# Optimization experiments

Hardware: AMD Instinct MI355X
Metric: run time of the kernel (lower is better)

Reference implementation:

```python
import jax, jax.numpy as jnp
import numpy as np

N = 100000        # nodes
E = 3200000       # edges per support (avg degree 32)
D_IN, D_OUT = 256, 128
ATT_H = 32
ALPHA, BETA = 0.5, 0.5  # FLAGS.alpha / FLAGS.beta


def setup_inputs() -> dict:
    key = jax.random.key(0)
    ks = jax.random.split(key, 10)
    x = jax.random.normal(ks[0], (N, D_IN), dtype=jnp.float32)
    glorot = lambda k, shp: jax.random.uniform(k, shp, jnp.float32,
                                               -np.sqrt(6.0 / sum(shp)), np.sqrt(6.0 / sum(shp)))
    Wa = glorot(ks[1], (D_IN, D_OUT))
    Wb = glorot(ks[2], (D_IN, D_OUT))
    Wc = glorot(ks[3], (D_IN, D_OUT))
    attn_w1 = glorot(ks[4], (D_OUT, ATT_H))
    attn_b1 = jnp.zeros((ATT_H,), jnp.float32)
    attn_w2 = glorot(ks[5], (ATT_H, 1))
    rows = jax.random.randint(ks[6], (7, E), 0, N, dtype=jnp.int32)
    cols = jax.random.randint(ks[7], (7, E), 0, N, dtype=jnp.int32)
    # normalized-adjacency-like positive values, scaled ~1/degree
    vals = jax.random.uniform(ks[8], (7, E), jnp.float32) * (1.0 / 32.0)
    return {"x": x, "Wa": Wa, "Wb": Wb, "Wc": Wc,
            "attn_w1": attn_w1, "attn_b1": attn_b1, "attn_w2": attn_w2,
            "rows": rows, "cols": cols, "vals": vals}


def reference(x, Wa, Wb, Wc, attn_w1, attn_b1, attn_w2, rows, cols, vals):
    n = x.shape[0]

    def spmm(i, X):
        # support[i] @ X via COO gather-scale-scatter: memory-bound SpMM
        return jax.ops.segment_sum(vals[i][:, None] * X[cols[i]], rows[i], num_segments=n)

    def bilinear_pooling(i, X):
        s = spmm(i, X)
        return 0.5 * (s * s - spmm(i, X * X))

    pre_a = x @ Wa                    # [N, D_OUT]
    pre_b = x @ Wb
    _ = x @ Wc                        # computed in original, never used
    sec_ord = 0.5 * (pre_a * pre_a - pre_a * pre_b)
    pre_al = pre_a + sec_ord

    emb = jnp.stack([pre_a, pre_al], axis=1)          # [N, 2, D_OUT]
    h = jnp.tanh(emb @ attn_w1 + attn_b1)             # [N, 2, 32]
    att = jax.nn.softmax(h @ attn_w2, axis=1)         # [N, 2, 1]
    pre_sup = jnp.sum(att * emb, axis=1)              # [N, D_OUT]

    out_gcn = spmm(0, pre_sup)
    out_bi1 = spmm(5, bilinear_pooling(1, pre_sup) - bilinear_pooling(3, pre_sup))
    out_bi2 = spmm(6, bilinear_pooling(2, pre_sup) - bilinear_pooling(4, pre_sup))
    out_bi = (1.0 - BETA) * out_bi1 + BETA * out_bi2
    output = (1.0 - ALPHA) * out_gcn + ALPHA * out_bi
    return jax.nn.relu(output)
```

## Files before the change

kernel.cpp:

```cpp
#include <hip/hip_runtime.h>

typedef unsigned int uint;
typedef unsigned short ushort;

__device__ __forceinline__ float bfl(uint u){ return __uint_as_float(u << 16); }
__device__ __forceinline__ float bfh(uint u){ return __uint_as_float(u & 0xFFFF0000u); }
__device__ __forceinline__ uint f2bfbits(float f){
    uint b = __float_as_uint(f);
    return (b + 0x7FFFu + ((b >> 16) & 1u)) >> 16;
}
__device__ __forceinline__ uint packbf2(float a, float b){
    return f2bfbits(a) | (f2bfbits(b) << 16);
}
__device__ __forceinline__ int smap(int4 m, int s){
    return (s == 0) ? m.x : (s == 1) ? m.y : (s == 2) ? m.z : m.w;
}
__device__ __forceinline__ int2 ldnt(const int2* p){
    long long v = __builtin_nontemporal_load((const long long*)p);
    int2 r; r.x = (int)(v & 0xFFFFFFFFll); r.y = (int)(v >> 32); return r;
}

#define CH 6144
#define SBSHIFT 7
#define SBROWS 128
#define HISTP 784
#define SBUF_CAP 5120
#define PGRID 2048


#define BM 64
#define BK 32
__global__ __launch_bounds__(256) void gemm_kernel(const float* __restrict__ x,
                                                   const float* __restrict__ Wa,
                                                   const float* __restrict__ Wb,
                                                   float* __restrict__ AB, int N) {
    __shared__ float xsT[BK][BM + 4];
    __shared__ float wsm[BK][256];
    int t = threadIdx.x;
    int rowbase = blockIdx.x * BM;
    int tx = t & 15, ty = t >> 4;
    float acc[4][16];
    #pragma unroll
    for (int i = 0; i < 4; i++)
        #pragma unroll
        for (int j = 0; j < 16; j++) acc[i][j] = 0.f;

    for (int k0 = 0; k0 < 256; k0 += BK) {
        {
            int r = t & 63;
            int koff = (t >> 6) * 8;
            int gr = rowbase + r; if (gr >= N) gr = N - 1;
            const float* src = x + (size_t)gr * 256 + k0 + koff;
            float4 u0 = *(const float4*)(src);
            float4 u1 = *(const float4*)(src + 4);
            xsT[koff + 0][r] = u0.x; xsT[koff + 1][r] = u0.y;
            xsT[koff + 2][r] = u0.z; xsT[koff + 3][r] = u0.w;
            xsT[koff + 4][r] = u1.x; xsT[koff + 5][r] = u1.y;
            xsT[koff + 6][r] = u1.z; xsT[koff + 7][r] = u1.w;
        }
        {
            #pragma unroll
            for (int i = 0; i < 8; i++) {
                int f = t + i * 256;
                int rr = f >> 6, c4 = f & 63;
                const float* src = (c4 < 32) ? &Wa[(size_t)(k0 + rr) * 128 + c4 * 4]
                                             : &Wb[(size_t)(k0 + rr) * 128 + (c4 - 32) * 4];
                *(float4*)&wsm[rr][c4 * 4] = *(const float4*)src;
            }
        }
        __syncthreads();
        #pragma unroll
        for (int kk = 0; kk < BK; ++kk) {
            float4 a = *(const float4*)&xsT[kk][ty * 4];
            float av[4] = {a.x, a.y, a.z, a.w};
            float bv[16];
            #pragma unroll
            for (int q = 0; q < 4; q++)
                *(float4*)&bv[q * 4] = *(const float4*)&wsm[kk][q * 64 + tx * 4];
            #pragma unroll
            for (int i = 0; i < 4; i++)
                #pragma unroll
                for (int j = 0; j < 16; j++)
                    acc[i][j] = fmaf(av[i], bv[j], acc[i][j]);
        }
        __syncthreads();
    }
    #pragma unroll
    for (int i = 0; i < 4; i++) {
        int gr = rowbase + ty * 4 + i;
        if (gr < N) {
            #pragma unroll
            for (int q = 0; q < 4; q++) {
                float4 o = {acc[i][q*4], acc[i][q*4+1], acc[i][q*4+2], acc[i][q*4+3]};
                *(float4*)&AB[(size_t)gr * 256 + q * 64 + tx * 4] = o;
            }
        }
    }
}

__global__ __launch_bounds__(256) void attn_kernel(const float* __restrict__ AB,
        const float* __restrict__ w1, const float* __restrict__ b1,
        const float* __restrict__ w2, uint* __restrict__ Pb, int N) {
    __shared__ float w1s[128 * 32];
    __shared__ float b1s[32], w2s[32];
    __shared__ float aS[4][128], alS[4][128];
    int t = threadIdx.x;
    #pragma unroll
    for (int i = 0; i < 16; i++) w1s[t + i * 256] = w1[t + i * 256];
    if (t < 32) { b1s[t] = b1[t]; w2s[t] = w2[t]; }

    int w = t >> 6, lane = t & 63;
    int node = blockIdx.x * 4 + w;
    bool active = node < N;
    int nclamp = active ? node : (N - 1);
    float2 a = *(const float2*)(AB + (size_t)nclamp * 256 + lane * 2);
    float2 b = *(const float2*)(AB + (size_t)nclamp * 256 + 128 + lane * 2);
    float2 al;
    al.x = a.x + 0.5f * (a.x * a.x - a.x * b.x);
    al.y = a.y + 0.5f * (a.y * a.y - a.y * b.y);
    aS[w][lane * 2] = a.x;   aS[w][lane * 2 + 1] = a.y;
    alS[w][lane * 2] = al.x; alS[w][lane * 2 + 1] = al.y;
    __syncthreads();

    int j = lane & 31;
    const float* src = (lane < 32) ? aS[w] : alS[w];
    float acc = b1s[j];
    #pragma unroll 8
    for (int d = 0; d < 128; ++d) acc = fmaf(src[d], w1s[d * 32 + j], acc);
    float h = tanhf(acc);
    float prod = h * w2s[j];
    #pragma unroll
    for (int off = 1; off < 32; off <<= 1) prod += __shfl_xor(prod, off);
    float eo = __shfl_xor(prod, 32);
    float e0 = (lane < 32) ? prod : eo;
    float e1 = (lane < 32) ? eo : prod;
    float m = fmaxf(e0, e1);
    float p0 = expf(e0 - m), p1 = expf(e1 - m);
    float inv = 1.0f / (p0 + p1);
    float at0 = p0 * inv, at1 = p1 * inv;
    if (active) {
        float px = at0 * a.x + at1 * al.x;
        float py = at0 * a.y + at1 * al.y;
        Pb[(size_t)node * 64 + lane] = packbf2(px, py);
    }
}


__device__ __forceinline__ void block_scan1024(int* a, int t, int* wsum) {
    int lane = t & 63, wid = t >> 6;
    int c0 = a[t * 4], c1 = a[t * 4 + 1], c2 = a[t * 4 + 2], c3 = a[t * 4 + 3];
    int tsum = c0 + c1 + c2 + c3, incl = tsum;
    #pragma unroll
    for (int off = 1; off < 64; off <<= 1) {
        int y = __shfl_up(incl, off);
        if (lane >= off) incl += y;
    }
    if (lane == 63) wsum[wid] = incl;
    __syncthreads();
    int wb = 0;
    #pragma unroll
    for (int w = 0; w < 4; w++) if (w < wid) wb += wsum[w];
    int excl = wb + incl - tsum;
    a[t * 4] = excl; a[t * 4 + 1] = excl + c0;
    a[t * 4 + 2] = excl + c0 + c1; a[t * 4 + 3] = excl + c0 + c1 + c2;
    __syncthreads();
}

__global__ __launch_bounds__(256) void count_chunk(const int* __restrict__ rows, int4 map,
        int* __restrict__ lenTab, int* __restrict__ gtot, int NSB, int nchunks, int E) {
    __shared__ int hist[HISTP];
    int c = blockIdx.x, s = blockIdx.y, t = threadIdx.x;
    size_t sb = (size_t)smap(map, s) * E;
    int e0 = c * CH, e1 = e0 + CH; if (e1 > E) e1 = E;
    for (int i = t; i < HISTP; i += 256) hist[i] = 0;
    __syncthreads();
    for (int e = e0 + t; e < e1; e += 256)
        atomicAdd(&hist[(uint)rows[sb + e] >> SBSHIFT], 1);
    __syncthreads();
    for (int b = t; b < NSB; b += 256) {
        int l = hist[b];
        lenTab[((size_t)s * NSB + b) * nchunks + c] = l;
        if (l) atomicAdd(&gtot[s * NSB + b], l);
    }
}

__global__ __launch_bounds__(256) void bucket_scanex(const int* __restrict__ gtot,
        int* __restrict__ bbase, int NSB) {
    __shared__ int a[1024];
    __shared__ int wsum[4];
    int s = blockIdx.x, t = threadIdx.x;
    #pragma unroll
    for (int k = 0; k < 4; k++) {
        int i = t + k * 256;
        a[i] = (i < NSB) ? gtot[s * NSB + i] : 0;
    }
    __syncthreads();
    block_scan1024(a, t, wsum);
    #pragma unroll
    for (int k = 0; k < 4; k++) {
        int i = t + k * 256;
        if (i <= NSB) bbase[s * (NSB + 1) + i] = a[i];
    }
}

__global__ __launch_bounds__(64) void pos_scan(const int* __restrict__ lenTab,
        const int* __restrict__ bbase, int* __restrict__ segPos, int NSB, int nchunks) {
    int b = blockIdx.x, s = blockIdx.y, lane = threadIdx.x;
    const int* lt = lenTab + ((size_t)s * NSB + b) * nchunks;
    int* sp = segPos + ((size_t)s * NSB + b) * nchunks;
    int run = bbase[s * (NSB + 1) + b];
    for (int c0 = 0; c0 < nchunks; c0 += 64) {
        int c = c0 + lane;
        int v = (c < nchunks) ? lt[c] : 0;
        int incl = v;
        #pragma unroll
        for (int off = 1; off < 64; off <<= 1) {
            int y = __shfl_up(incl, off);
            if (lane >= off) incl += y;
        }
        if (c < nchunks) sp[c] = run + incl - v;
        run += __shfl(incl, 63);
    }
}

__global__ __launch_bounds__(256) void place_chunk(const int* __restrict__ rows,
        const int* __restrict__ cols, const float* __restrict__ vals, int4 map,
        const int* __restrict__ segPos, int2* __restrict__ stage2,
        int NSB, int nchunks, int E) {
    __shared__ int2 sbuf[CH];
    __shared__ ushort bmap[CH];
    __shared__ int cur[1024];
    __shared__ int off[1024];
    __shared__ int spos[HISTP];
    __shared__ int wsum[4];
    int c = blockIdx.x, s = blockIdx.y, t = threadIdx.x;
    size_t sb = (size_t)smap(map, s) * E;
    int e0 = c * CH, e1 = e0 + CH; if (e1 > E) e1 = E;
    int csz = e1 - e0;
    #pragma unroll
    for (int k = 0; k < 4; k++) cur[t + k * 256] = 0;
    __syncthreads();
    for (int e = e0 + t; e < e1; e += 256)
        atomicAdd(&cur[(uint)rows[sb + e] >> SBSHIFT], 1);
    __syncthreads();
    block_scan1024(cur, t, wsum);
    #pragma unroll
    for (int k = 0; k < 4; k++) { int i = t + k * 256; off[i] = cur[i]; }
    for (int b = t; b < NSB; b += 256)
        spos[b] = segPos[((size_t)s * NSB + b) * nchunks + c];
    __syncthreads();
    for (int e = e0 + t; e < e1; e += 256) {
        int r = rows[sb + e];
        int b = (uint)r >> SBSHIFT;
        int pos = atomicAdd(&cur[b], 1);
        uint cw = (uint)cols[sb + e] | ((uint)(r & (SBROWS - 1)) << 20);
        sbuf[pos] = make_int2((int)cw, __float_as_int(vals[sb + e]));
        bmap[pos] = (ushort)b;
    }
    __syncthreads();
    int2* dst = stage2 + (size_t)s * E;
    for (int i = t; i < csz; i += 256) {
        int b = bmap[i];
        dst[spos[b] + (i - off[b])] = sbuf[i];
    }
}

__global__ __launch_bounds__(256) void fill_bucket(const int2* __restrict__ stage2,
        const int* __restrict__ bbase, int* __restrict__ rp, int2* __restrict__ pk,
        int NSB, int N, int E) {
    __shared__ int2 sbuf[SBUF_CAP];
    __shared__ int cur[128];
    __shared__ int loc[132];
    __shared__ int wsum2[2];
    int b = blockIdx.x, s = blockIdx.y, t = threadIdx.x;
    int lane = t & 63, wid = t >> 6;
    int rowbase = b << SBSHIFT;
    int nrows = N - rowbase; if (nrows > SBROWS) nrows = SBROWS;
    size_t sb = (size_t)s * E;
    int beg = bbase[s * (NSB + 1) + b];
    int end = bbase[s * (NSB + 1) + b + 1];
    int tot = end - beg;
    if (t < 128) cur[t] = 0;
    __syncthreads();
    for (int i = beg + t; i < end; i += 256)
        atomicAdd(&cur[((uint)stage2[sb + i].x) >> 20], 1);
    __syncthreads();
    int v = 0, incl = 0;
    if (t < 128) {
        v = cur[t]; incl = v;
        #pragma unroll
        for (int off = 1; off < 64; off <<= 1) {
            int y = __shfl_up(incl, off);
            if (lane >= off) incl += y;
        }
        if (lane == 63) wsum2[wid] = incl;
    }
    __syncthreads();
    if (t < 128) {
        int excl = incl - v + ((wid == 1) ? wsum2[0] : 0);
        loc[t] = excl; cur[t] = excl;
        if (t < nrows) rp[(size_t)s * (N + 1) + rowbase + t] = beg + excl;
    }
    if (t == 0) loc[128] = tot;
    if (b == 0 && t == 0) rp[(size_t)s * (N + 1) + N] = E;
    __syncthreads();
    for (int i = beg + t; i < end; i += 256) {
        int2 u = stage2[sb + i];
        int lr = ((uint)u.x) >> 20;
        int pos = atomicAdd(&cur[lr], 1);
        int2 w = make_int2(u.x & 0xFFFFF, u.y);
        if (pos < SBUF_CAP) sbuf[pos] = w; else pk[sb + beg + pos] = w;
    }
    __syncthreads();
    for (int r = wid; r < nrows; r += 4) {
        int rb = loc[r], re = loc[r + 1];
        int deg = re - rb;
        if (deg < 2 || deg > 64 || re > SBUF_CAP) continue;
        int key = 0x7FFFFFFF, val = 0;
        if (lane < deg) { int2 u = sbuf[rb + lane]; key = u.x; val = u.y; }
        #pragma unroll
        for (int k = 2; k <= 64; k <<= 1) {
            #pragma unroll
            for (int j = k >> 1; j > 0; j >>= 1) {
                int okey = __shfl_xor(key, j);
                int oval = __shfl_xor(val, j);
                bool up = ((lane & k) == 0);
                bool lower = ((lane & j) == 0);
                bool keepmin = (lower == up);
                bool take = keepmin ? (okey < key) : (okey > key);
                if (take) { key = okey; val = oval; }
            }
        }
        if (lane < deg) sbuf[rb + lane] = make_int2(key, val);
    }
    __syncthreads();
    int lim = (tot < SBUF_CAP) ? tot : SBUF_CAP;
    for (int i = t; i < lim; i += 256)
        __builtin_nontemporal_store(*(const long long*)&sbuf[i], (long long*)&pk[sb + beg + i]);
}


__device__ __forceinline__ void row_gather_sum(const int2* __restrict__ pk,
        int e, int end, const uint* __restrict__ Xb, int lane,
        float& ax, float& ay) {
    for (; e + 4 <= end; e += 4) {
        int2 c0 = ldnt(&pk[e]);     int2 c1 = ldnt(&pk[e + 1]);
        int2 c2 = ldnt(&pk[e + 2]); int2 c3 = ldnt(&pk[e + 3]);
        uint u0 = Xb[(c0.x << 6) + lane]; uint u1 = Xb[(c1.x << 6) + lane];
        uint u2 = Xb[(c2.x << 6) + lane]; uint u3 = Xb[(c3.x << 6) + lane];
        float v0 = __int_as_float(c0.y), v1 = __int_as_float(c1.y);
        float v2 = __int_as_float(c2.y), v3 = __int_as_float(c3.y);
        ax = fmaf(v0, bfl(u0), ax); ay = fmaf(v0, bfh(u0), ay);
        ax = fmaf(v1, bfl(u1), ax); ay = fmaf(v1, bfh(u1), ay);
        ax = fmaf(v2, bfl(u2), ax); ay = fmaf(v2, bfh(u2), ay);
        ax = fmaf(v3, bfl(u3), ax); ay = fmaf(v3, bfh(u3), ay);
    }
    for (; e < end; ++e) {
        int2 c0 = ldnt(&pk[e]);
        uint u0 = Xb[(c0.x << 6) + lane];
        float v0 = __int_as_float(c0.y);
        ax = fmaf(v0, bfl(u0), ax); ay = fmaf(v0, bfh(u0), ay);
    }
}

__device__ __forceinline__ void row_gather_bp(const int2* __restrict__ pk,
        int e, int end, const uint* __restrict__ Xb, int lane,
        float& sx, float& sy, float& qx, float& qy) {
    for (; e + 4 <= end; e += 4) {
        int2 c0 = ldnt(&pk[e]);     int2 c1 = ldnt(&pk[e + 1]);
        int2 c2 = ldnt(&pk[e + 2]); int2 c3 = ldnt(&pk[e + 3]);
        uint u0 = Xb[(c0.x << 6) + lane]; uint u1 = Xb[(c1.x << 6) + lane];
        uint u2 = Xb[(c2.x << 6) + lane]; uint u3 = Xb[(c3.x << 6) + lane];
        float v0 = __int_as_float(c0.y), v1 = __int_as_float(c1.y);
        float v2 = __int_as_float(c2.y), v3 = __int_as_float(c3.y);
        float x0 = bfl(u0), y0 = bfh(u0), x1 = bfl(u1), y1 = bfh(u1);
        float x2 = bfl(u2), y2 = bfh(u2), x3 = bfl(u3), y3 = bfh(u3);
        sx = fmaf(v0, x0, sx); sy = fmaf(v0, y0, sy);
        qx = fmaf(v0 * x0, x0, qx); qy = fmaf(v0 * y0, y0, qy);
        sx = fmaf(v1, x1, sx); sy = fmaf(v1, y1, sy);
        qx = fmaf(v1 * x1, x1, qx); qy = fmaf(v1 * y1, y1, qy);
        sx = fmaf(v2, x2, sx); sy = fmaf(v2, y2, sy);
        qx = fmaf(v2 * x2, x2, qx); qy = fmaf(v2 * y2, y2, qy);
        sx = fmaf(v3, x3, sx); sy = fmaf(v3, y3, sy);
        qx = fmaf(v3 * x3, x3, qx); qy = fmaf(v3 * y3, y3, qy);
    }
    for (; e < end; ++e) {
        int2 c0 = ldnt(&pk[e]);
        uint u0 = Xb[(c0.x << 6) + lane];
        float v0 = __int_as_float(c0.y);
        float x0 = bfl(u0), y0 = bfh(u0);
        sx = fmaf(v0, x0, sx); sy = fmaf(v0, y0, sy);
        qx = fmaf(v0 * x0, x0, qx); qy = fmaf(v0 * y0, y0, qy);
    }
}

__global__ __launch_bounds__(256) void spmm_bp2(const int* __restrict__ rpA,
        const int2* __restrict__ pkA, const int* __restrict__ rpB,
        const int2* __restrict__ pkB, const uint* __restrict__ Xb,
        uint* __restrict__ outb, int N) {
    int w = threadIdx.x >> 6, lane = threadIdx.x & 63;
    int stride = gridDim.x * 4;
    for (int row = blockIdx.x * 4 + w; row < N; row += stride) {
        float sax = 0.f, say = 0.f, qax = 0.f, qay = 0.f;
        float sbx = 0.f, sby = 0.f, qbx = 0.f, qby = 0.f;
        row_gather_bp(pkA, rpA[row], rpA[row + 1], Xb, lane, sax, say, qax, qay);
        row_gather_bp(pkB, rpB[row], rpB[row + 1], Xb, lane, sbx, sby, qbx, qby);
        float tx = 0.5f * ((sax * sax - qax) - (sbx * sbx - qbx));
        float ty = 0.5f * ((say * say - qay) - (sby * sby - qby));
        outb[((size_t)row << 6) + lane] = packbf2(tx, ty);
    }
}

__global__ __launch_bounds__(256) void spmm_out(const int* __restrict__ rp0,
        const int2* __restrict__ pk0, const int* __restrict__ rp5,
        const int2* __restrict__ pk5, const int* __restrict__ rp6,
        const int2* __restrict__ pk6, const uint* __restrict__ Pb,
        const uint* __restrict__ t1b, const uint* __restrict__ t2b,
        float* __restrict__ out, int N) {
    int w = threadIdx.x >> 6, lane = threadIdx.x & 63;
    int stride = gridDim.x * 4;
    for (int row = blockIdx.x * 4 + w; row < N; row += stride) {
        float a0x = 0.f, a0y = 0.f, a5x = 0.f, a5y = 0.f, a6x = 0.f, a6y = 0.f;
        row_gather_sum(pk0, rp0[row], rp0[row + 1], Pb,  lane, a0x, a0y);
        row_gather_sum(pk5, rp5[row], rp5[row + 1], t1b, lane, a5x, a5y);
        row_gather_sum(pk6, rp6[row], rp6[row + 1], t2b, lane, a6x, a6y);
        float rx = fmaxf(0.5f * a0x + 0.25f * a5x + 0.25f * a6x, 0.f);
        float ry = fmaxf(0.5f * a0y + 0.25f * a5y + 0.25f * a6y, 0.f);
        *(float2*)(out + ((size_t)row << 7) + (lane << 1)) = make_float2(rx, ry);
    }
}


extern "C" void kernel_launch(void* const* d_in, const int* in_sizes, int n_in,
                              void* d_out, int out_size, void* d_ws, size_t ws_size,
                              hipStream_t stream) {
    (void)n_in; (void)out_size; (void)ws_size;
    const float* x   = (const float*)d_in[0];
    const float* Wa  = (const float*)d_in[1];
    const float* Wb  = (const float*)d_in[2];
    const float* w1  = (const float*)d_in[4];
    const float* b1  = (const float*)d_in[5];
    const float* w2  = (const float*)d_in[6];
    const int* rows  = (const int*)d_in[7];
    const int* cols  = (const int*)d_in[8];
    const float* vals = (const float*)d_in[9];
    float* out = (float*)d_out;

    const int N = in_sizes[0] / 256;
    const int E = in_sizes[7] / 7;
    const int NSB = (N + SBROWS - 1) >> SBSHIFT;
    const int nchunks = (E + CH - 1) / CH;

    uint* Pb  = (uint*)d_ws;
    uint* t1b = Pb + (size_t)N * 64;
    uint* t2b = t1b + (size_t)N * 64;
    int2* pk  = (int2*)(t2b + (size_t)N * 64);
    size_t regionFloats = (size_t)N * 256;
    if ((size_t)8 * E > regionFloats) regionFloats = (size_t)8 * E;
    int2* stage2 = pk + (size_t)4 * E;
    float* AB    = (float*)stage2;
    int* rp      = (int*)((float*)stage2 + regionFloats);
    int* lenTab  = rp + 4 * (size_t)(N + 1);
    int* segPos  = lenTab + (size_t)4 * NSB * nchunks;
    int* gtot    = segPos + (size_t)4 * NSB * nchunks;
    int* bbase   = gtot + (size_t)4 * NSB;

    dim3 b256(256);
    int sgrid = (N + 3) / 4;
    int pgrid = PGRID; if (pgrid > sgrid) pgrid = sgrid;

    gemm_kernel<<<(N + BM - 1) / BM, b256, 0, stream>>>(x, Wa, Wb, AB, N);
    attn_kernel<<<sgrid, b256, 0, stream>>>(AB, w1, b1, w2, Pb, N);

    auto build = [&](int4 map, int nsup) {
        hipMemsetAsync(gtot, 0, (size_t)nsup * NSB * sizeof(int), stream);
        count_chunk<<<dim3(nchunks, nsup), b256, 0, stream>>>(rows, map, lenTab, gtot,
                                                              NSB, nchunks, E);
        bucket_scanex<<<nsup, b256, 0, stream>>>(gtot, bbase, NSB);
        pos_scan<<<dim3(NSB, nsup), dim3(64), 0, stream>>>(lenTab, bbase, segPos, NSB, nchunks);
        place_chunk<<<dim3(nchunks, nsup), b256, 0, stream>>>(rows, cols, vals, map,
                                                              segPos, stage2, NSB, nchunks, E);
        fill_bucket<<<dim3(NSB, nsup), b256, 0, stream>>>(stage2, bbase, rp, pk, NSB, N, E);
    };

    const int NP1 = N + 1;

    build(make_int4(1, 3, 2, 4), 4);
    spmm_bp2<<<pgrid, b256, 0, stream>>>(rp + 0 * NP1, pk + 0 * (size_t)E,
                                         rp + 1 * NP1, pk + 1 * (size_t)E, Pb, t1b, N);
    spmm_bp2<<<pgrid, b256, 0, stream>>>(rp + 2 * NP1, pk + 2 * (size_t)E,
                                         rp + 3 * NP1, pk + 3 * (size_t)E, Pb, t2b, N);

    build(make_int4(0, 5, 6, 6), 3);
    spmm_out<<<pgrid, b256, 0, stream>>>(rp + 0 * NP1, pk + 0 * (size_t)E,
                                         rp + 1 * NP1, pk + 1 * (size_t)E,
                                         rp + 2 * NP1, pk + 2 * (size_t)E,
                                         Pb, t1b, t2b, out, N);
}
```

Before: 2.212 ms.

## Fuse four bilinear SpMMs into one kernel with interleaved gathers

Merges the two spmm_bp2 launches into a single spmm_bp4 kernel that processes supports 1-4 together for each row. The four edge lists (and the three lists in spmm_out) are walked in lockstep, two edges at a time each, so many independent gathers are in flight at once. This targets memory latency on the random row gathers and saves one launch. The cost is higher register pressure from sixteen accumulators, and the per-list unroll drops from 4 to 2.

```diff
diff --git a/kernel.cpp b/kernel.cpp
--- a/kernel.cpp
+++ b/kernel.cpp
@@ -26,6 +26,16 @@
 #define HISTP 784
 #define SBUF_CAP 5120
 #define PGRID 2048
+
+#define ACCBP(sx,sy,qx,qy,cv,u) { \
+    float v_ = __int_as_float((cv).y); \
+    float xx_ = bfl(u), yy_ = bfh(u); \
+    sx = fmaf(v_, xx_, sx); sy = fmaf(v_, yy_, sy); \
+    qx = fmaf(v_ * xx_, xx_, qx); qy = fmaf(v_ * yy_, yy_, qy); }
+
+#define ACCS(ax,ay,cv,u) { \
+    float v_ = __int_as_float((cv).y); \
+    ax = fmaf(v_, bfl(u), ax); ay = fmaf(v_, bfh(u), ay); }
 
 
 #define BM 64
@@ -343,71 +353,76 @@
 __device__ __forceinline__ void row_gather_sum(const int2* __restrict__ pk,
         int e, int end, const uint* __restrict__ Xb, int lane,
         float& ax, float& ay) {
-    for (; e + 4 <= end; e += 4) {
-        int2 c0 = ldnt(&pk[e]);     int2 c1 = ldnt(&pk[e + 1]);
-        int2 c2 = ldnt(&pk[e + 2]); int2 c3 = ldnt(&pk[e + 3]);
+    for (; e + 2 <= end; e += 2) {
+        int2 c0 = ldnt(&pk[e]); int2 c1 = ldnt(&pk[e + 1]);
         uint u0 = Xb[(c0.x << 6) + lane]; uint u1 = Xb[(c1.x << 6) + lane];
-        uint u2 = Xb[(c2.x << 6) + lane]; uint u3 = Xb[(c3.x << 6) + lane];
-        float v0 = __int_as_float(c0.y), v1 = __int_as_float(c1.y);
-        float v2 = __int_as_float(c2.y), v3 = __int_as_float(c3.y);
-        ax = fmaf(v0, bfl(u0), ax); ay = fmaf(v0, bfh(u0), ay);
-        ax = fmaf(v1, bfl(u1), ax); ay = fmaf(v1, bfh(u1), ay);
-        ax = fmaf(v2, bfl(u2), ax); ay = fmaf(v2, bfh(u2), ay);
-        ax = fmaf(v3, bfl(u3), ax); ay = fmaf(v3, bfh(u3), ay);
-    }
-    for (; e < end; ++e) {
+        ACCS(ax, ay, c0, u0); ACCS(ax, ay, c1, u1);
+    }
+    if (e < end) {
         int2 c0 = ldnt(&pk[e]);
         uint u0 = Xb[(c0.x << 6) + lane];
-        float v0 = __int_as_float(c0.y);
-        ax = fmaf(v0, bfl(u0), ax); ay = fmaf(v0, bfh(u0), ay);
+        ACCS(ax, ay, c0, u0);
     }
 }
 
 __device__ __forceinline__ void row_gather_bp(const int2* __restrict__ pk,
         int e, int end, const uint* __restrict__ Xb, int lane,
         float& sx, float& sy, float& qx, float& qy) {
-    for (; e + 4 <= end; e += 4) {
-        int2 c0 = ldnt(&pk[e]);     int2 c1 = ldnt(&pk[e + 1]);
-        int2 c2 = ldnt(&pk[e + 2]); int2 c3 = ldnt(&pk[e + 3]);
+    for (; e + 2 <= end; e += 2) {
+        int2 c0 = ldnt(&pk[e]); int2 c1 = ldnt(&pk[e + 1]);
         uint u0 = Xb[(c0.x << 6) + lane]; uint u1 = Xb[(c1.x << 6) + lane];
-        uint u2 = Xb[(c2.x << 6) + lane]; uint u3 = Xb[(c3.x << 6) + lane];
-        float v0 = __int_as_float(c0.y), v1 = __int_as_float(c1.y);
-        float v2 = __int_as_float(c2.y), v3 = __int_as_float(c3.y);
-        float x0 = bfl(u0), y0 = bfh(u0), x1 = bfl(u1), y1 = bfh(u1);
-        float x2 = bfl(u2), y2 = bfh(u2), x3 = bfl(u3), y3 = bfh(u3);
-        sx = fmaf(v0, x0, sx); sy = fmaf(v0, y0, sy);
-        qx = fmaf(v0 * x0, x0, qx); qy = fmaf(v0 * y0, y0, qy);
-        sx = fmaf(v1, x1, sx); sy = fmaf(v1, y1, sy);
-        qx = fmaf(v1 * x1, x1, qx); qy = fmaf(v1 * y1, y1, qy);
-        sx = fmaf(v2, x2, sx); sy = fmaf(v2, y2, sy);
-        qx = fmaf(v2 * x2, x2, qx); qy = fmaf(v2 * y2, y2, qy);
-        sx = fmaf(v3, x3, sx); sy = fmaf(v3, y3, sy);
-        qx = fmaf(v3 * x3, x3, qx); qy = fmaf(v3 * y3, y3, qy);
-    }
-    for (; e < end; ++e) {
+        ACCBP(sx, sy, qx, qy, c0, u0); ACCBP(sx, sy, qx, qy, c1, u1);
+    }
+    if (e < end) {
         int2 c0 = ldnt(&pk[e]);
         uint u0 = Xb[(c0.x << 6) + lane];
-        float v0 = __int_as_float(c0.y);
-        float x0 = bfl(u0), y0 = bfh(u0);
-        sx = fmaf(v0, x0, sx); sy = fmaf(v0, y0, sy);
-        qx = fmaf(v0 * x0, x0, qx); qy = fmaf(v0 * y0, y0, qy);
-    }
-}
-
-__global__ __launch_bounds__(256) void spmm_bp2(const int* __restrict__ rpA,
-        const int2* __restrict__ pkA, const int* __restrict__ rpB,
-        const int2* __restrict__ pkB, const uint* __restrict__ Xb,
-        uint* __restrict__ outb, int N) {
+        ACCBP(sx, sy, qx, qy, c0, u0);
+    }
+}
+
+__global__ __launch_bounds__(256) void spmm_bp4(const int* __restrict__ rp1,
+        const int2* __restrict__ pk1, const int* __restrict__ rp2,
+        const int2* __restrict__ pk2, const int* __restrict__ rp3,
+        const int2* __restrict__ pk3, const int* __restrict__ rp4,
+        const int2* __restrict__ pk4, const uint* __restrict__ Xb,
+        uint* __restrict__ out1, uint* __restrict__ out2, int N) {
     int w = threadIdx.x >> 6, lane = threadIdx.x & 63;
     int stride = gridDim.x * 4;
     for (int row = blockIdx.x * 4 + w; row < N; row += stride) {
-        float sax = 0.f, say = 0.f, qax = 0.f, qay = 0.f;
-        float sbx = 0.f, sby = 0.f, qbx = 0.f, qby = 0.f;
-        row_gather_bp(pkA, rpA[row], rpA[row + 1], Xb, lane, sax, say, qax, qay);
-        row_gather_bp(pkB, rpB[row], rpB[row + 1], Xb, lane, sbx, sby, qbx, qby);
-        float tx = 0.5f * ((sax * sax - qax) - (sbx * sbx - qbx));
-        float ty = 0.5f * ((say * say - qay) - (sby * sby - qby));
-        outb[((size_t)row << 6) + lane] = packbf2(tx, ty);
+        float s1x=0.f,s1y=0.f,q1x=0.f,q1y=0.f;
+        float s2x=0.f,s2y=0.f,q2x=0.f,q2y=0.f;
+        float s3x=0.f,s3y=0.f,q3x=0.f,q3y=0.f;
+        float s4x=0.f,s4y=0.f,q4x=0.f,q4y=0.f;
+        int e1 = rp1[row], n1 = rp1[row + 1];
+        int e2 = rp2[row], n2 = rp2[row + 1];
+        int e3 = rp3[row], n3 = rp3[row + 1];
+        int e4 = rp4[row], n4 = rp4[row + 1];
+        while (e1 + 2 <= n1 && e2 + 2 <= n2 && e3 + 2 <= n3 && e4 + 2 <= n4) {
+            int2 a0 = ldnt(&pk1[e1]); int2 a1 = ldnt(&pk1[e1 + 1]);
+            int2 b0 = ldnt(&pk2[e2]); int2 b1 = ldnt(&pk2[e2 + 1]);
+            int2 c0 = ldnt(&pk3[e3]); int2 c1 = ldnt(&pk3[e3 + 1]);
+            int2 d0 = ldnt(&pk4[e4]); int2 d1 = ldnt(&pk4[e4 + 1]);
+            uint ua0 = Xb[(a0.x << 6) + lane]; uint ua1 = Xb[(a1.x << 6) + lane];
+            uint ub0 = Xb[(b0.x << 6) + lane]; uint ub1 = Xb[(b1.x << 6) + lane];
+            uint uc0 = Xb[(c0.x << 6) + lane]; uint uc1 = Xb[(c1.x << 6) + lane];
+            uint ud0 = Xb[(d0.x << 6) + lane]; uint ud1 = Xb[(d1.x << 6) + lane];
+            ACCBP(s1x,s1y,q1x,q1y,a0,ua0); ACCBP(s1x,s1y,q1x,q1y,a1,ua1);
+            ACCBP(s2x,s2y,q2x,q2y,b0,ub0); ACCBP(s2x,s2y,q2x,q2y,b1,ub1);
+            ACCBP(s3x,s3y,q3x,q3y,c0,uc0); ACCBP(s3x,s3y,q3x,q3y,c1,uc1);
+            ACCBP(s4x,s4y,q4x,q4y,d0,ud0); ACCBP(s4x,s4y,q4x,q4y,d1,ud1);
+            e1 += 2; e2 += 2; e3 += 2; e4 += 2;
+        }
+        row_gather_bp(pk1, e1, n1, Xb, lane, s1x, s1y, q1x, q1y);
+        row_gather_bp(pk2, e2, n2, Xb, lane, s2x, s2y, q2x, q2y);
+        row_gather_bp(pk3, e3, n3, Xb, lane, s3x, s3y, q3x, q3y);
+        row_gather_bp(pk4, e4, n4, Xb, lane, s4x, s4y, q4x, q4y);
+        float t1x = 0.5f * ((s1x * s1x - q1x) - (s2x * s2x - q2x));
+        float t1y = 0.5f * ((s1y * s1y - q1y) - (s2y * s2y - q2y));
+        float t2xv = 0.5f * ((s3x * s3x - q3x) - (s4x * s4x - q4x));
+        float t2yv = 0.5f * ((s3y * s3y - q3y) - (s4y * s4y - q4y));
+        size_t o = ((size_t)row << 6) + lane;
+        out1[o] = packbf2(t1x, t1y);
+        out2[o] = packbf2(t2xv, t2yv);
     }
 }
 
@@ -421,9 +436,24 @@
     int stride = gridDim.x * 4;
     for (int row = blockIdx.x * 4 + w; row < N; row += stride) {
         float a0x = 0.f, a0y = 0.f, a5x = 0.f, a5y = 0.f, a6x = 0.f, a6y = 0.f;
-        row_gather_sum(pk0, rp0[row], rp0[row + 1], Pb,  lane, a0x, a0y);
-        row_gather_sum(pk5, rp5[row], rp5[row + 1], t1b, lane, a5x, a5y);
-        row_gather_sum(pk6, rp6[row], rp6[row + 1], t2b, lane, a6x, a6y);
+        int e0 = rp0[row], n0 = rp0[row + 1];
+        int e5 = rp5[row], n5 = rp5[row + 1];
+        int e6 = rp6[row], n6 = rp6[row + 1];
+        while (e0 + 2 <= n0 && e5 + 2 <= n5 && e6 + 2 <= n6) {
+            int2 c00 = ldnt(&pk0[e0]); int2 c01 = ldnt(&pk0[e0 + 1]);
+            int2 c50 = ldnt(&pk5[e5]); int2 c51 = ldnt(&pk5[e5 + 1]);
+            int2 c60 = ldnt(&pk6[e6]); int2 c61 = ldnt(&pk6[e6 + 1]);
+            uint u00 = Pb[(c00.x << 6) + lane];  uint u01 = Pb[(c01.x << 6) + lane];
+            uint u50 = t1b[(c50.x << 6) + lane]; uint u51 = t1b[(c51.x << 6) + lane];
+            uint u60 = t2b[(c60.x << 6) + lane]; uint u61 = t2b[(c61.x << 6) + lane];
+            ACCS(a0x, a0y, c00, u00); ACCS(a0x, a0y, c01, u01);
+            ACCS(a5x, a5y, c50, u50); ACCS(a5x, a5y, c51, u51);
+            ACCS(a6x, a6y, c60, u60); ACCS(a6x, a6y, c61, u61);
+            e0 += 2; e5 += 2; e6 += 2;
+        }
+        row_gather_sum(pk0, e0, n0, Pb,  lane, a0x, a0y);
+        row_gather_sum(pk5, e5, n5, t1b, lane, a5x, a5y);
+        row_gather_sum(pk6, e6, n6, t2b, lane, a6x, a6y);
         float rx = fmaxf(0.5f * a0x + 0.25f * a5x + 0.25f * a6x, 0.f);
         float ry = fmaxf(0.5f * a0y + 0.25f * a5y + 0.25f * a6y, 0.f);
         *(float2*)(out + ((size_t)row << 7) + (lane << 1)) = make_float2(rx, ry);
@@ -486,10 +516,11 @@
     const int NP1 = N + 1;
 
     build(make_int4(1, 3, 2, 4), 4);
-    spmm_bp2<<<pgrid, b256, 0, stream>>>(rp + 0 * NP1, pk + 0 * (size_t)E,
-                                         rp + 1 * NP1, pk + 1 * (size_t)E, Pb, t1b, N);
-    spmm_bp2<<<pgrid, b256, 0, stream>>>(rp + 2 * NP1, pk + 2 * (size_t)E,
-                                         rp + 3 * NP1, pk + 3 * (size_t)E, Pb, t2b, N);
+    spmm_bp4<<<pgrid, b256, 0, stream>>>(rp + 0 * NP1, pk + 0 * (size_t)E,
+                                         rp + 1 * NP1, pk + 1 * (size_t)E,
+                                         rp + 2 * NP1, pk + 2 * (size_t)E,
+                                         rp + 3 * NP1, pk + 3 * (size_t)E,
+                                         Pb, t1b, t2b, N);
 
     build(make_int4(0, 5, 6, 6), 3);
     spmm_out<<<pgrid, b256, 0, stream>>>(rp + 0 * NP1, pk + 0 * (size_t)E,
```

After: 2.455 ms. 1.11x slower.
